# Performance work log

Measured on AMD Instinct MI355X. Metric: run time of the kernel, lower is better.

Reference implementation:

```python
import jax, jax.numpy as jnp
import numpy as np

NUM_GROUPS = 32
EPS = 1e-5
HEAD_DIM = 64

def group_norm(x, w, b):
    # x: [B,C,H,W]; normalize within 32 groups over (C//32, H, W)
    B, C, H, W = x.shape
    xg = x.reshape(B, NUM_GROUPS, C // NUM_GROUPS, H, W)
    mu = xg.mean(axis=(2, 3, 4), keepdims=True)
    var = xg.var(axis=(2, 3, 4), keepdims=True)
    xn = ((xg - mu) / jnp.sqrt(var + EPS)).reshape(B, C, H, W)
    return xn * w[None, :, None, None] + b[None, :, None, None]

def conv1x1(x, w, b):
    # w: [Cout, Cin], b: [Cout]
    return jnp.einsum('bchw,oc->bohw', x, w) + b[None, :, None, None]

def setup_inputs() -> dict:
    key = jax.random.key(0)
    ks = jax.random.split(key, 12)
    B, C, Cc, H, W = 16, 512, 512, 32, 32
    s = 0.02
    return {
        'x': jax.random.normal(ks[0], (B, C, H, W), jnp.float32),
        'context': jax.random.normal(ks[1], (B, Cc, H, W), jnp.float32),
        'norm_q_w': jnp.ones((C,), jnp.float32),
        'norm_q_b': jnp.zeros((C,), jnp.float32),
        'norm_kv_w': jnp.ones((Cc,), jnp.float32),
        'norm_kv_b': jnp.zeros((Cc,), jnp.float32),
        'conv_q_w': jax.random.normal(ks[2], (C, C), jnp.float32) * s,
        'conv_q_b': jnp.zeros((C,), jnp.float32),
        'conv_kv_w': jax.random.normal(ks[3], (2 * C, Cc), jnp.float32) * s,
        'conv_kv_b': jnp.zeros((2 * C,), jnp.float32),
        'proj_w': jax.random.normal(ks[4], (C, C), jnp.float32) * s,
        'proj_b': jnp.zeros((C,), jnp.float32),
    }

def reference(x, context, norm_q_w, norm_q_b, norm_kv_w, norm_kv_b,
              conv_q_w, conv_q_b, conv_kv_w, conv_kv_b, proj_w, proj_b):
    B, C, H, W = x.shape
    nh = max(1, C // HEAD_DIM)
    hd = C // nh
    q = conv1x1(group_norm(x, norm_q_w, norm_q_b), conv_q_w, conv_q_b)
    kv = conv1x1(group_norm(context, norm_kv_w, norm_kv_b), conv_kv_w, conv_kv_b)
    k, v = jnp.split(kv, 2, axis=1)
    L = H * W
    q = q.reshape(B, nh, hd, L)
    k = k.reshape(B, nh, hd, L)
    v = v.reshape(B, nh, hd, L)
    attn = jnp.einsum('bhdi,bhdj->bhij', q, k) * (hd ** -0.5)
    attn = jax.nn.softmax(attn, axis=-1)
    out = jnp.einsum('bhij,bhdj->bhdi', attn, v)
    return x + conv1x1(out.reshape(B, C, H, W), proj_w, proj_b)
```

## Files before the change

### kernel.cpp

```cpp
#include <hip/hip_runtime.h>
#include <hip/hip_bf16.h>

typedef short v8s __attribute__((ext_vector_type(8)));
typedef float v4f __attribute__((ext_vector_type(4)));
typedef float v16f __attribute__((ext_vector_type(16)));
typedef __hip_bfloat16 bf16;

__device__ __forceinline__ float b2f(bf16 h) { return __bfloat162float(h); }
__device__ __forceinline__ bf16 f2b(float f) { return __float2bfloat16(f); }

#define QSCALE 0.18033688f

__device__ __forceinline__ void gll16(const void* g, void* l) {
    __builtin_amdgcn_global_load_lds(
        (const __attribute__((address_space(1))) void*)g,
        (__attribute__((address_space(3))) void*)l, 16, 0, 0);
}

__device__ __forceinline__ unsigned cvtpk(float lo, float hi_) {
    unsigned r;
    asm("v_cvt_pk_bf16_f32 %0, %1, %2" : "=v"(r) : "v"(lo), "v"(hi_));
    return r;
}

__device__ __forceinline__ void pl32swap(unsigned& a, unsigned& b) {
    asm("v_permlane32_swap_b32 %0, %1" : "+v"(a), "+v"(b));
}

__global__ __launch_bounds__(256) void gn_t_kernel(
    const float* __restrict__ x, const float* __restrict__ ctx,
    const float* __restrict__ qw, const float* __restrict__ qb,
    const float* __restrict__ kw, const float* __restrict__ kb,
    bf16* __restrict__ xnT, bf16* __restrict__ cnT)
{
    const int b = blockIdx.y, g = blockIdx.x, z = blockIdx.z, c0 = g * 16;
    const float* src = z ? ctx : x;
    const float* gw  = z ? kw : qw;
    const float* gb  = z ? kb : qb;
    bf16* dst = z ? cnT : xnT;
    __shared__ __attribute__((aligned(16))) bf16 lx[16][1032];
    __shared__ float rS[4], rQ[4];
    __shared__ float sSc[16], sSh[16];
    const int t = threadIdx.x, wave = t >> 6, lane = t & 63;
    const float* xb = src + ((long)b * 512 + c0) * 1024;
    float sum = 0.f, sq = 0.f;
#pragma unroll
    for (int i = 0; i < 16; i++) {
        int q = t + i * 256;
        int ci = q >> 8, l0 = (q & 255) * 4;
        float4 v = *(const float4*)(xb + (long)ci * 1024 + l0);
        sum += v.x + v.y + v.z + v.w;
        sq  += v.x * v.x + v.y * v.y + v.z * v.z + v.w * v.w;
        union { short4 s4v; bf16 h[4]; } w;
        w.h[0] = f2b(v.x); w.h[1] = f2b(v.y); w.h[2] = f2b(v.z); w.h[3] = f2b(v.w);
        *(short4*)&lx[ci][l0] = w.s4v;
    }
#pragma unroll
    for (int off = 32; off > 0; off >>= 1) {
        sum += __shfl_down(sum, off);
        sq  += __shfl_down(sq, off);
    }
    if (lane == 0) { rS[wave] = sum; rQ[wave] = sq; }
    __syncthreads();
    if (t < 16) {
        float S = rS[0] + rS[1] + rS[2] + rS[3];
        float Q = rQ[0] + rQ[1] + rQ[2] + rQ[3];
        const float inv_n = 1.f / 16384.f;
        float mean = S * inv_n;
        float var  = Q * inv_n - mean * mean;
        float rstd = rsqrtf(var + 1e-5f);
        float w = gw[c0 + t];
        sSc[t] = rstd * w;
        sSh[t] = gb[c0 + t] - mean * rstd * w;
    }
    __syncthreads();
#pragma unroll
    for (int i = 0; i < 8; i++) {
        int p = t + i * 256;
        int l = p >> 1, half = (p & 1) * 8;
        union { float4 f4; bf16 h[8]; } o_;
#pragma unroll
        for (int j = 0; j < 8; j++) {
            float y = b2f(lx[half + j][l]) * sSc[half + j] + sSh[half + j];
            o_.h[j] = f2b(y);
        }
        *(float4*)(dst + ((long)b * 1024 + l) * 512 + c0 + half) = o_.f4;
    }
}

__global__ __launch_bounds__(256) void wconv_kernel(
    const float* __restrict__ a, const float* __restrict__ bsrc,
    const float* __restrict__ csrc, bf16* __restrict__ oa,
    bf16* __restrict__ ob, bf16* __restrict__ oc)
{
    int id = blockIdx.x * 256 + threadIdx.x;
    const float* src; bf16* dst; int off;
    if (id < 65536)       { src = a;    dst = oa; off = id; }
    else if (id < 196608) { src = bsrc; dst = ob; off = id - 65536; }
    else                  { src = csrc; dst = oc; off = id - 196608; }
    float4 v = ((const float4*)src)[off];
    union { short4 s4v; bf16 h[4]; } w;
    w.h[0] = f2b(v.x); w.h[1] = f2b(v.y); w.h[2] = f2b(v.z); w.h[3] = f2b(v.w);
    ((short4*)dst)[off] = w.s4v;
}

__global__ __launch_bounds__(256) void qkv_gemm_kernel(
    const bf16* __restrict__ xnT, const bf16* __restrict__ cnT,
    const bf16* __restrict__ wQ, const bf16* __restrict__ wKV,
    bf16* __restrict__ QT, bf16* __restrict__ KT, bf16* __restrict__ Vo,
    const float* __restrict__ cqb, const float* __restrict__ ckvb)
{
    const long PB = 512L * 1024;
    const int z = blockIdx.z, op = z >> 4, bz = z & 15;
    const bf16* A; const bf16* B; bf16* C; const float* bias;
    int nBlkN, N, biasPerM; float scale;
    if (op == 0) {
        A = xnT + bz * PB; B = wQ;  C = QT + bz * PB; bias = cqb;
        nBlkN = 4; N = 512; biasPerM = 0; scale = QSCALE;
    } else if (op == 1) {
        A = cnT + bz * PB; B = wKV; C = KT + bz * PB; bias = ckvb;
        nBlkN = 4; N = 512; biasPerM = 0; scale = 1.0f;
    } else {
        A = wKV + 512L * 512; B = cnT + bz * PB; C = Vo + bz * PB; bias = ckvb + 512;
        nBlkN = 8; N = 1024; biasPerM = 1; scale = 1.0f;
    }
    const int bx = blockIdx.x;
    const int m0 = (bx / nBlkN) * 128, n0 = (bx % nBlkN) * 128;
    __shared__ __attribute__((aligned(16))) bf16 lA[128][64];
    __shared__ __attribute__((aligned(16))) bf16 lB[128][64];
    const int t = threadIdx.x, wave = t >> 6, lane = t & 63;
    const int quad = lane >> 4, c = lane & 15;
    const int wm = (wave >> 1) * 64, wn = (wave & 1) * 64;
    const int rIS = lane >> 3;
    const int chG = (lane & 7) ^ rIS;
    const bf16* Ag[4]; const bf16* Bg[4];
    bf16* Al[4]; bf16* Bl[4];
#pragma unroll
    for (int j = 0; j < 4; j++) {
        int seg = wave + j * 4;
        int row = seg * 8 + rIS;
        Ag[j] = A + (long)(m0 + row) * 512 + chG * 8;
        Bg[j] = B + (long)(n0 + row) * 512 + chG * 8;
        Al[j] = &lA[seg * 8][0];
        Bl[j] = &lB[seg * 8][0];
    }
    v4f acc[4][4] = {};
    for (int k0 = 0; k0 < 512; k0 += 64) {
        __syncthreads();
#pragma unroll
        for (int j = 0; j < 4; j++) {
            gll16(Ag[j] + k0, Al[j]);
            gll16(Bg[j] + k0, Bl[j]);
        }
        __syncthreads();
#pragma unroll
        for (int kk = 0; kk < 2; kk++) {
            v8s af[4], bfr[4];
#pragma unroll
            for (int mt = 0; mt < 4; mt++)
                af[mt] = *(const v8s*)&lA[wm + mt * 16 + c][((kk * 4 + quad) ^ (c & 7)) * 8];
#pragma unroll
            for (int nt = 0; nt < 4; nt++)
                bfr[nt] = *(const v8s*)&lB[wn + nt * 16 + c][((kk * 4 + quad) ^ (c & 7)) * 8];
#pragma unroll
            for (int mt = 0; mt < 4; mt++)
#pragma unroll
                for (int nt = 0; nt < 4; nt++)
                    acc[mt][nt] = __builtin_amdgcn_mfma_f32_16x16x32_bf16(
                        af[mt], bfr[nt], acc[mt][nt], 0, 0, 0);
        }
    }
#pragma unroll
    for (int mt = 0; mt < 4; mt++) {
#pragma unroll
        for (int nt = 0; nt < 4; nt++) {
#pragma unroll
            for (int r = 0; r < 4; r++) {
                int row = m0 + wm + mt * 16 + quad * 4 + r;
                int col = n0 + wn + nt * 16 + c;
                float v = (acc[mt][nt][r] + (biasPerM ? bias[row] : bias[col])) * scale;
                C[(long)row * N + col] = f2b(v);
            }
        }
    }
}

__global__ __launch_bounds__(256) void gemm_proj_kernel(
    const bf16* __restrict__ A,
    const bf16* __restrict__ B, long sBb,
    float* __restrict__ C,
    const float* __restrict__ bias,
    const float* __restrict__ resid,
    int M, int N)
{
    const int bz = blockIdx.z;
    const int m0 = blockIdx.x * 128, n0 = blockIdx.y * 128;
    const bf16* Bb = B + (long)bz * sBb;
    __shared__ __attribute__((aligned(16))) bf16 lA[128][64];
    __shared__ __attribute__((aligned(16))) bf16 lB[128][64];
    const int t = threadIdx.x, wave = t >> 6, lane = t & 63;
    const int quad = lane >> 4, c = lane & 15;
    const int wm = (wave >> 1) * 64, wn = (wave & 1) * 64;
    const int rIS = lane >> 3, chG = (lane & 7) ^ rIS;
    const bf16* Ag[4]; const bf16* Bg[4];
    bf16* Al[4]; bf16* Bl[4];
#pragma unroll
    for (int j = 0; j < 4; j++) {
        int seg = wave + j * 4;
        int row = seg * 8 + rIS;
        Ag[j] = A + (long)(m0 + row) * 512 + chG * 8;
        Bg[j] = Bb + (long)(n0 + row) * 512 + chG * 8;
        Al[j] = &lA[seg * 8][0];
        Bl[j] = &lB[seg * 8][0];
    }
    v4f acc[4][4] = {};
    for (int k0 = 0; k0 < 512; k0 += 64) {
        __syncthreads();
#pragma unroll
        for (int j = 0; j < 4; j++) {
            gll16(Ag[j] + k0, Al[j]);
            gll16(Bg[j] + k0, Bl[j]);
        }
        __syncthreads();
#pragma unroll
        for (int kk = 0; kk < 2; kk++) {
            v8s af[4], bfr[4];
#pragma unroll
            for (int mt = 0; mt < 4; mt++)
                af[mt] = *(const v8s*)&lA[wm + mt * 16 + c][((kk * 4 + quad) ^ (c & 7)) * 8];
#pragma unroll
            for (int nt = 0; nt < 4; nt++)
                bfr[nt] = *(const v8s*)&lB[wn + nt * 16 + c][((kk * 4 + quad) ^ (c & 7)) * 8];
#pragma unroll
            for (int mt = 0; mt < 4; mt++)
#pragma unroll
                for (int nt = 0; nt < 4; nt++)
                    acc[mt][nt] = __builtin_amdgcn_mfma_f32_16x16x32_bf16(
                        af[mt], bfr[nt], acc[mt][nt], 0, 0, 0);
        }
    }
#pragma unroll
    for (int mt = 0; mt < 4; mt++) {
#pragma unroll
        for (int nt = 0; nt < 4; nt++) {
#pragma unroll
            for (int r = 0; r < 4; r++) {
                int row = m0 + wm + mt * 16 + quad * 4 + r;
                int col = n0 + wn + nt * 16 + c;
                float v = acc[mt][nt][r] + bias[row]
                        + resid[(long)bz * ((long)M * N) + (long)row * N + col];
                C[(long)bz * ((long)M * N) + (long)row * N + col] = v;
            }
        }
    }
}

__global__ __launch_bounds__(256, 2) void attn_kernel(
    const bf16* QT, const bf16* __restrict__ KT,
    const bf16* __restrict__ V, bf16* AOT)
{
    const int nblk = blockIdx.x;
    const int s = nblk >> 3;
    const int it = s & 3;
    const int g = ((s >> 2) << 3) | (nblk & 7);
    const int h = g & 7, b = g >> 3;
    const int i0 = it * 256;
    __shared__ __attribute__((aligned(16))) bf16 lk[3][64][64];
    __shared__ __attribute__((aligned(16))) bf16 lv[3][64][64];
    const int t = threadIdx.x, wave = t >> 6, lane = t & 63;
    const int m31 = lane & 31, hi = lane >> 5;
    const int rIS = lane >> 3, chG = (lane & 7) ^ rIS;
    v8s qf[2][4];
#pragma unroll
    for (int iq = 0; iq < 2; iq++) {
        const bf16* Qb = QT + ((long)b * 1024 + i0 + wave * 64 + iq * 32 + m31) * 512 + h * 64;
#pragma unroll
        for (int ks = 0; ks < 4; ks++)
            qf[iq][ks] = *(const v8s*)(Qb + ks * 16 + hi * 8);
    }
    const bf16* Kg[2]; const bf16* Vg[2];
#pragma unroll
    for (int j = 0; j < 2; j++) {
        int seg = wave * 2 + j;
        Kg[j] = KT + ((long)b * 1024 + seg * 8 + rIS) * 512 + h * 64 + chG * 8;
        Vg[j] = V + ((long)b * 512 + h * 64 + seg * 8 + rIS) * 1024 + chG * 8;
    }
    auto issue = [&](int jtx, int bi) {
#pragma unroll
        for (int j = 0; j < 2; j++) {
            int seg = wave * 2 + j;
            gll16(Kg[j] + (long)jtx * 64 * 512, &lk[bi][seg * 8][0]);
            gll16(Vg[j] + (long)jtx * 64,      &lv[bi][seg * 8][0]);
        }
    };
    issue(0, 0);
    issue(1, 1);
    float lsum0 = 0.f, lsum1 = 0.f;
    v16f o00 = {}, o01 = {}, o10 = {}, o11 = {};

#define SMPV(sj0, sj1, JB)                                                     \
    {                                                                          \
        unsigned u0[8], u1[8];                                                 \
        _Pragma("unroll")                                                      \
        for (int k2 = 0; k2 < 8; k2++) {                                       \
            float p0l = __builtin_amdgcn_exp2f(sj0[2 * k2]);                   \
            float p0h = __builtin_amdgcn_exp2f(sj0[2 * k2 + 1]);               \
            float p1l = __builtin_amdgcn_exp2f(sj1[2 * k2]);                   \
            float p1h = __builtin_amdgcn_exp2f(sj1[2 * k2 + 1]);               \
            lsum0 += p0l + p0h; lsum1 += p1l + p1h;                            \
            u0[k2] = cvtpk(p0l, p0h); u1[k2] = cvtpk(p1l, p1h);                \
        }                                                                      \
        pl32swap(u0[0], u0[2]); pl32swap(u0[1], u0[3]);                        \
        pl32swap(u0[4], u0[6]); pl32swap(u0[5], u0[7]);                        \
        pl32swap(u1[0], u1[2]); pl32swap(u1[1], u1[3]);                        \
        pl32swap(u1[4], u1[6]); pl32swap(u1[5], u1[7]);                        \
        __builtin_amdgcn_s_setprio(1);                                         \
        _Pragma("unroll")                                                      \
        for (int kk = 0; kk < 2; kk++) {                                       \
            union { unsigned w[4]; v8s v; } pf0, pf1;                          \
            pf0.w[0] = u0[4 * kk + 0]; pf0.w[1] = u0[4 * kk + 1];              \
            pf0.w[2] = u0[4 * kk + 2]; pf0.w[3] = u0[4 * kk + 3];              \
            pf1.w[0] = u1[4 * kk + 0]; pf1.w[1] = u1[4 * kk + 1];              \
            pf1.w[2] = u1[4 * kk + 2]; pf1.w[3] = u1[4 * kk + 3];              \
            const int cc2 = ((JB) * 2 + kk) * 2 + hi;                          \
            v8s vf0 = *(const v8s*)&lv[cur][m31][(cc2 ^ (m31 & 7)) * 8];       \
            o00 = __builtin_amdgcn_mfma_f32_32x32x16_bf16(vf0, pf0.v, o00, 0, 0, 0); \
            o10 = __builtin_amdgcn_mfma_f32_32x32x16_bf16(vf0, pf1.v, o10, 0, 0, 0); \
            v8s vf1 = *(const v8s*)&lv[cur][32 + m31][(cc2 ^ (m31 & 7)) * 8];  \
            o01 = __builtin_amdgcn_mfma_f32_32x32x16_bf16(vf1, pf0.v, o01, 0, 0, 0); \
            o11 = __builtin_amdgcn_mfma_f32_32x32x16_bf16(vf1, pf1.v, o11, 0, 0, 0); \
        }                                                                      \
        __builtin_amdgcn_s_setprio(0);                                         \
    }

    for (int jt = 0; jt < 16; jt++) {
        const int cur = jt % 3;
        asm volatile("s_waitcnt vmcnt(4)" ::: "memory");
        __builtin_amdgcn_s_barrier();
        __builtin_amdgcn_sched_barrier(0);
        issue((jt + 2) & 15, (jt + 2) % 3);
        v16f s00 = {}, s01 = {}, s10 = {}, s11 = {};
        __builtin_amdgcn_s_setprio(1);
#pragma unroll
        for (int ks = 0; ks < 4; ks++) {
            const int chs = ((ks * 2 + hi) ^ (m31 & 7)) * 8;
            v8s kf0 = *(const v8s*)&lk[cur][m31][chs];
            v8s kf1 = *(const v8s*)&lk[cur][32 + m31][chs];
            s00 = __builtin_amdgcn_mfma_f32_32x32x16_bf16(kf0, qf[0][ks], s00, 0, 0, 0);
            s01 = __builtin_amdgcn_mfma_f32_32x32x16_bf16(kf0, qf[1][ks], s01, 0, 0, 0);
            s10 = __builtin_amdgcn_mfma_f32_32x32x16_bf16(kf1, qf[0][ks], s10, 0, 0, 0);
            s11 = __builtin_amdgcn_mfma_f32_32x32x16_bf16(kf1, qf[1][ks], s11, 0, 0, 0);
        }
        __builtin_amdgcn_s_setprio(0);
        SMPV(s00, s01, 0)
        SMPV(s10, s11, 1)
    }
#undef SMPV
    {
        float lt0 = lsum0 + __shfl_xor(lsum0, 32);
        float lt1 = lsum1 + __shfl_xor(lsum1, 32);
        float inv0 = 1.f / lt0, inv1 = 1.f / lt1;
#pragma unroll
        for (int iq = 0; iq < 2; iq++) {
            float inv = iq ? inv1 : inv0;
            const v16f& oa = iq ? o10 : o00;
            const v16f& ob = iq ? o11 : o01;
            bf16* Ob = AOT + ((long)b * 1024 + i0 + wave * 64 + iq * 32 + m31) * 512 + h * 64;
#pragma unroll
            for (int gq = 0; gq < 4; gq++) {
                union { short4 s4v; bf16 hh[4]; } w0, w1;
#pragma unroll
                for (int k = 0; k < 4; k++) {
                    w0.hh[k] = f2b(oa[gq * 4 + k] * inv);
                    w1.hh[k] = f2b(ob[gq * 4 + k] * inv);
                }
                *(short4*)(Ob + gq * 8 + hi * 4)      = w0.s4v;
                *(short4*)(Ob + 32 + gq * 8 + hi * 4) = w1.s4v;
            }
        }
    }
}

extern "C" void kernel_launch(void* const* d_in, const int* in_sizes, int n_in,
                              void* d_out, int out_size, void* d_ws, size_t ws_size,
                              hipStream_t stream)
{
    const float* x    = (const float*)d_in[0];
    const float* ctx  = (const float*)d_in[1];
    const float* nqw  = (const float*)d_in[2];
    const float* nqb  = (const float*)d_in[3];
    const float* nkw  = (const float*)d_in[4];
    const float* nkb  = (const float*)d_in[5];
    const float* cqw  = (const float*)d_in[6];
    const float* cqb  = (const float*)d_in[7];
    const float* ckvw = (const float*)d_in[8];
    const float* ckvb = (const float*)d_in[9];
    const float* pw   = (const float*)d_in[10];
    const float* pb   = (const float*)d_in[11];
    float* out = (float*)d_out;
    bf16* ws  = (bf16*)d_ws;

    const long PB  = 512L * 1024;
    const long TOT = 16L * PB;
    bf16* s0 = ws;
    bf16* s1 = ws + TOT;
    bf16* s2 = ws + 2 * TOT;
    bf16* s3 = ws + 3 * TOT;
    bf16* s4 = ws + 4 * TOT;
    bf16* wQ  = ws + 5 * TOT;
    bf16* wKV = wQ + 262144;
    bf16* wP  = wKV + 524288;

    dim3 blk(256);
    gn_t_kernel<<<dim3(32, 16, 2), blk, 0, stream>>>(
        x, ctx, nqw, nqb, nkw, nkb, s0, s1);
    wconv_kernel<<<dim3(1024), blk, 0, stream>>>(cqw, ckvw, pw, wQ, wKV, wP);
    qkv_gemm_kernel<<<dim3(32, 1, 48), blk, 0, stream>>>(
        s0, s1, wQ, wKV, s2, s3, s4, cqb, ckvb);
    attn_kernel<<<dim3(512), blk, 0, stream>>>(s2, s3, s4, s2);
    gemm_proj_kernel<<<dim3(4, 8, 16), blk, 0, stream>>>(
        wP, s2, PB, out, pb, x, 512, 1024);
}
```

Measured before the change: 237.5 us.

## Double-buffer LDS tiles in QKV GEMM and remap blocks by XCD

The QKV GEMM now keeps two LDS buffers and issues async global-to-LDS loads for the next k-tile while computing on the current one, with one barrier per iteration instead of two. The grid is flattened to 1D and remapped so blocks on the same XCD share batch indices, which should improve L2 locality for operands of the same batch. This doubles LDS use per block, which may lower occupancy.

```diff
diff --git a/kernel.cpp b/kernel.cpp
--- a/kernel.cpp
+++ b/kernel.cpp
@@ -111,7 +111,11 @@
     const float* __restrict__ cqb, const float* __restrict__ ckvb)
 {
     const long PB = 512L * 1024;
-    const int z = blockIdx.z, op = z >> 4, bz = z & 15;
+    const int blk = blockIdx.x;
+    const int xcd = blk & 7, idx = blk >> 3;
+    const int half = idx / 96, rr = idx % 96;
+    const int op = rr >> 5, bx = rr & 31;
+    const int bz = xcd + 8 * half;
     const bf16* A; const bf16* B; bf16* C; const float* bias;
     int nBlkN, N, biasPerM; float scale;
     if (op == 0) {
@@ -124,44 +128,46 @@
         A = wKV + 512L * 512; B = cnT + bz * PB; C = Vo + bz * PB; bias = ckvb + 512;
         nBlkN = 8; N = 1024; biasPerM = 1; scale = 1.0f;
     }
-    const int bx = blockIdx.x;
     const int m0 = (bx / nBlkN) * 128, n0 = (bx % nBlkN) * 128;
-    __shared__ __attribute__((aligned(16))) bf16 lA[128][64];
-    __shared__ __attribute__((aligned(16))) bf16 lB[128][64];
+    __shared__ __attribute__((aligned(16))) bf16 lA[2][128][64];
+    __shared__ __attribute__((aligned(16))) bf16 lB[2][128][64];
     const int t = threadIdx.x, wave = t >> 6, lane = t & 63;
     const int quad = lane >> 4, c = lane & 15;
     const int wm = (wave >> 1) * 64, wn = (wave & 1) * 64;
     const int rIS = lane >> 3;
     const int chG = (lane & 7) ^ rIS;
-    const bf16* Ag[4]; const bf16* Bg[4];
-    bf16* Al[4]; bf16* Bl[4];
+    const bf16* Ag[4]; const bf16* Bg[4]; int segr[4];
 #pragma unroll
     for (int j = 0; j < 4; j++) {
         int seg = wave + j * 4;
-        int row = seg * 8 + rIS;
-        Ag[j] = A + (long)(m0 + row) * 512 + chG * 8;
-        Bg[j] = B + (long)(n0 + row) * 512 + chG * 8;
-        Al[j] = &lA[seg * 8][0];
-        Bl[j] = &lB[seg * 8][0];
-    }
+        segr[j] = seg * 8;
+        Ag[j] = A + (long)(m0 + segr[j] + rIS) * 512 + chG * 8;
+        Bg[j] = B + (long)(n0 + segr[j] + rIS) * 512 + chG * 8;
+    }
+    auto issue = [&](int k0, int bi) {
+#pragma unroll
+        for (int j = 0; j < 4; j++) {
+            gll16(Ag[j] + k0, &lA[bi][segr[j]][0]);
+            gll16(Bg[j] + k0, &lB[bi][segr[j]][0]);
+        }
+    };
     v4f acc[4][4] = {};
-    for (int k0 = 0; k0 < 512; k0 += 64) {
-        __syncthreads();
-#pragma unroll
-        for (int j = 0; j < 4; j++) {
-            gll16(Ag[j] + k0, Al[j]);
-            gll16(Bg[j] + k0, Bl[j]);
-        }
-        __syncthreads();
+    issue(0, 0);
+    for (int kc = 0; kc < 8; kc++) {
+        const int cur = kc & 1;
+        asm volatile("s_waitcnt vmcnt(0)" ::: "memory");
+        __builtin_amdgcn_s_barrier();
+        __builtin_amdgcn_sched_barrier(0);
+        if (kc < 7) issue((kc + 1) * 64, cur ^ 1);
 #pragma unroll
         for (int kk = 0; kk < 2; kk++) {
             v8s af[4], bfr[4];
 #pragma unroll
             for (int mt = 0; mt < 4; mt++)
-                af[mt] = *(const v8s*)&lA[wm + mt * 16 + c][((kk * 4 + quad) ^ (c & 7)) * 8];
+                af[mt] = *(const v8s*)&lA[cur][wm + mt * 16 + c][((kk * 4 + quad) ^ (c & 7)) * 8];
 #pragma unroll
             for (int nt = 0; nt < 4; nt++)
-                bfr[nt] = *(const v8s*)&lB[wn + nt * 16 + c][((kk * 4 + quad) ^ (c & 7)) * 8];
+                bfr[nt] = *(const v8s*)&lB[cur][wn + nt * 16 + c][((kk * 4 + quad) ^ (c & 7)) * 8];
 #pragma unroll
             for (int mt = 0; mt < 4; mt++)
 #pragma unroll
@@ -415,7 +421,7 @@
     gn_t_kernel<<<dim3(32, 16, 2), blk, 0, stream>>>(
         x, ctx, nqw, nqb, nkw, nkb, s0, s1);
     wconv_kernel<<<dim3(1024), blk, 0, stream>>>(cqw, ckvw, pw, wQ, wKV, wP);
-    qkv_gemm_kernel<<<dim3(32, 1, 48), blk, 0, stream>>>(
+    qkv_gemm_kernel<<<dim3(1536), blk, 0, stream>>>(
         s0, s1, wQ, wKV, s2, s3, s4, cqb, ckvb);
     attn_kernel<<<dim3(512), blk, 0, stream>>>(s2, s3, s4, s2);
     gemm_proj_kernel<<<dim3(4, 8, 16), blk, 0, stream>>>(
```

Result: no change. 240.1 us (+1.1%).
